# Optimization experiments

Hardware: AMD Instinct MI355X
Metric: run time of the kernel (lower is better)

## Reference

```python
import jax, jax.numpy as jnp
import numpy as np

B, L, D, E = 32, 2048, 1024, 2048

def setup_inputs() -> dict:
    key = jax.random.key(0)
    k1, k2, k3, k4, k5 = jax.random.split(key, 5)
    scale_s = 1.0 / np.sqrt(D)
    scale_h = 1.0 / np.sqrt(E)
    return {
        "dec_hidden": jax.random.normal(k1, (B, D), jnp.float32),
        "enc_outputs": jax.random.normal(k2, (B, L, E), jnp.float32),
        "W_s": jax.random.normal(k3, (D, D), jnp.float32) * scale_s,
        "W_h": jax.random.normal(k4, (D, E), jnp.float32) * scale_h,
        "v": jax.random.normal(k5, (D,), jnp.float32) * scale_s,
    }

def reference(dec_hidden, enc_outputs, W_s, W_h, v):
    # s: [B, D] -- projected decoder state (broadcast over src_len, no repeat)
    s = jnp.einsum('bd,ed->be', dec_hidden, W_s)
    # h: [B, L, D] -- projected encoder outputs
    h = jnp.einsum('ble,de->bld', enc_outputs, W_h)
    # additive scores: v^T tanh(s + h) -> [B, L]
    scores = jnp.einsum('bld,d->bl', jnp.tanh(s[:, None, :] + h), v)
    attn = jax.nn.softmax(scores, axis=1)
    # context: weighted sum of encoder outputs -> [B, E]
    ctx = jnp.einsum('bl,ble->be', attn, enc_outputs)
    return (ctx, attn)
```

## Files before the change

### kernel.cpp

```cpp
#include <hip/hip_runtime.h>
#include <cstdint>
#include <cstddef>

#define B_ 32
#define L_ 2048
#define D_ 1024
#define E_ 2048

typedef __attribute__((ext_vector_type(8))) short short8;
typedef __attribute__((ext_vector_type(16))) float f32x16;
typedef __attribute__((ext_vector_type(4))) unsigned int uint4v;

__device__ __forceinline__ void async_copy16(const void* g, void* l) {
  __builtin_amdgcn_global_load_lds((const __attribute__((address_space(1))) void*)g,
                                   (__attribute__((address_space(3))) void*)l, 16, 0, 0);
}

__device__ __forceinline__ unsigned int pack_bf16_2(float lo, float hi) {
  unsigned int ul = __builtin_bit_cast(unsigned int, lo) + 0x8000u;
  unsigned int uh = __builtin_bit_cast(unsigned int, hi) + 0x8000u;
  return (ul >> 16) | (uh & 0xFFFF0000u);
}

__device__ __forceinline__ float fast_tanh(float x) {
  float e = __expf(2.0f * x);
  return 1.0f - 2.0f / (e + 1.0f);
}

__global__ __launch_bounds__(256) void k_s(const float* __restrict__ dec,
                                           const float* __restrict__ Ws,
                                           float* __restrict__ s) {
  int wid = threadIdx.x >> 6, lane = threadIdx.x & 63;
  int out = blockIdx.x * 4 + wid;
  int b = out >> 10, i = out & 1023;
  const float* dr = dec + b * D_;
  const float* wr = Ws + (size_t)i * D_;
  float acc = 0.f;
#pragma unroll
  for (int c = 0; c < 4; ++c) {
    int d0 = c * 256 + lane * 4;
    float4 x = *(const float4*)(dr + d0);
    float4 w = *(const float4*)(wr + d0);
    acc += x.x * w.x + x.y * w.y + x.z * w.z + x.w * w.w;
  }
#pragma unroll
  for (int off = 32; off >= 1; off >>= 1) acc += __shfl_xor(acc, off, 64);
  if (lane == 0) s[out] = acc;
}

__global__ __launch_bounds__(256) void k_cvt(const float* __restrict__ src,
                                             unsigned short* __restrict__ dst) {
  size_t i = ((size_t)blockIdx.x * 256 + threadIdx.x) * 8;
  float4 a = *(const float4*)(src + i);
  float4 b = *(const float4*)(src + i + 4);
  uint4v p;
  p.x = pack_bf16_2(a.x, a.y);
  p.y = pack_bf16_2(a.z, a.w);
  p.z = pack_bf16_2(b.x, b.y);
  p.w = pack_bf16_2(b.z, b.w);
  *(uint4v*)(dst + i) = p;
}

__global__ __launch_bounds__(256, 3) void k_gemm(const float* __restrict__ enc,
                                                 const unsigned short* __restrict__ whb,
                                                 const float* __restrict__ sbias,
                                                 const float* __restrict__ vvec,
                                                 float* __restrict__ scores) {
  __shared__ alignas(16) float As[128 * 64];
  __shared__ alignas(16) unsigned short Bs[64 * 128];

  const int tid = threadIdx.x;
  const int wid = tid >> 6;
  const int lane = tid & 63;
  const int wm = wid >> 1;
  const int wn = wid & 1;

  const int flat = blockIdx.x;
  const int nt = (flat >> 3) & 7;
  const int mt = (flat & 7) | ((flat >> 6) << 3);
  const int m_base = mt * 128, n_base = nt * 128;
  const int b_idx = m_base >> 11;

  const int rp = lane >> 4;
  const int ul = lane & 15;
  const int u0 = ul ^ rp;
  const float* gA = enc + (size_t)(m_base + wid * 32 + rp) * E_;
  int offA[8];
#pragma unroll
  for (int it = 0; it < 8; ++it)
    offA[it] = it * 4 * E_ + ((u0 ^ ((it & 3) << 2)) << 2);
  const unsigned short* gB = whb + (size_t)n_base * E_;
  int offB[4];
#pragma unroll
  for (int it = 0; it < 4; ++it) {
    int ulog = u0 ^ (it << 2);
    offB[it] = (wid * 32 + it * 8 + 2 * rp + (ulog >> 3)) * E_ + (ulog & 7) * 8;
  }

  const int col = lane & 31;
  const int h = lane >> 5;
  const float* arow[2];
#pragma unroll
  for (int mi = 0; mi < 2; ++mi) arow[mi] = &As[(wm * 64 + mi * 32 + col) * 64];
  int aoff[4][2];
#pragma unroll
  for (int ks = 0; ks < 4; ++ks)
#pragma unroll
    for (int j = 0; j < 2; ++j)
      aoff[ks][j] = ((ks * 4 + h * 2 + j) ^ (col & 15)) * 4;
  const unsigned short* brow[2];
#pragma unroll
  for (int ni = 0; ni < 2; ++ni) brow[ni] = &Bs[(wn * 32 + ni * 16 + (col >> 1)) * 128];
  int boff[4];
#pragma unroll
  for (int ks = 0; ks < 4; ++ks)
    boff[ks] = ((((col & 1) << 3) + ks * 2 + h) ^ ((col >> 1) & 15)) * 8;

  f32x16 acc[2][2] = {};

  for (int kk = 0; kk < E_; kk += 64) {
    __syncthreads();
#pragma unroll
    for (int it = 0; it < 8; ++it)
      async_copy16(gA + offA[it] + kk, &As[(wid * 32 + it * 4) * 64]);
#pragma unroll
    for (int it = 0; it < 4; ++it)
      async_copy16(gB + offB[it] + kk, &Bs[(wid * 16 + it * 4) * 128]);
    __syncthreads();

#pragma unroll
    for (int ks = 0; ks < 4; ++ks) {
      short8 bf[2];
#pragma unroll
      for (int ni = 0; ni < 2; ++ni) bf[ni] = *(const short8*)(brow[ni] + boff[ks]);
#pragma unroll
      for (int mi = 0; mi < 2; ++mi) {
        float4 f0 = *(const float4*)(arow[mi] + aoff[ks][0]);
        float4 f1 = *(const float4*)(arow[mi] + aoff[ks][1]);
        uint4v pa;
        pa.x = pack_bf16_2(f0.x, f0.y);
        pa.y = pack_bf16_2(f0.z, f0.w);
        pa.z = pack_bf16_2(f1.x, f1.y);
        pa.w = pack_bf16_2(f1.z, f1.w);
        short8 af = __builtin_bit_cast(short8, pa);
#pragma unroll
        for (int ni = 0; ni < 2; ++ni)
          acc[mi][ni] = __builtin_amdgcn_mfma_f32_32x32x16_bf16(af, bf[ni], acc[mi][ni], 0, 0, 0);
      }
    }
  }

  float vv[2], sv[2];
#pragma unroll
  for (int ni = 0; ni < 2; ++ni) {
    int n = n_base + wn * 64 + ni * 32 + col;
    vv[ni] = vvec[n];
    sv[ni] = sbias[b_idx * D_ + n];
  }
#pragma unroll
  for (int mi = 0; mi < 2; ++mi) {
#pragma unroll
    for (int reg = 0; reg < 16; ++reg) {
      float sum = 0.f;
#pragma unroll
      for (int ni = 0; ni < 2; ++ni)
        sum += vv[ni] * fast_tanh(sv[ni] + acc[mi][ni][reg]);
      sum += __shfl_xor(sum, 1, 64);
      sum += __shfl_xor(sum, 2, 64);
      sum += __shfl_xor(sum, 4, 64);
      sum += __shfl_xor(sum, 8, 64);
      sum += __shfl_xor(sum, 16, 64);
      if (col == 0)
        atomicAdd(&scores[m_base + wm * 64 + mi * 32 + (reg & 3) + 8 * (reg >> 2) + h * 4], sum);
    }
  }
}

__global__ __launch_bounds__(256) void k_softmax(float* __restrict__ sc) {
  int b = blockIdx.x, tid = threadIdx.x;
  int lane = tid & 63, wid = tid >> 6;
  float* row = sc + (size_t)b * L_;
  float vals[8];
  float mx = -1e30f;
#pragma unroll
  for (int j = 0; j < 8; ++j) { vals[j] = row[tid + j * 256]; mx = fmaxf(mx, vals[j]); }
#pragma unroll
  for (int off = 32; off >= 1; off >>= 1) mx = fmaxf(mx, __shfl_xor(mx, off, 64));
  __shared__ float redm[4], reds[4];
  if (lane == 0) redm[wid] = mx;
  __syncthreads();
  mx = fmaxf(fmaxf(redm[0], redm[1]), fmaxf(redm[2], redm[3]));
  float sum = 0.f;
#pragma unroll
  for (int j = 0; j < 8; ++j) { vals[j] = __expf(vals[j] - mx); sum += vals[j]; }
#pragma unroll
  for (int off = 32; off >= 1; off >>= 1) sum += __shfl_xor(sum, off, 64);
  if (lane == 0) reds[wid] = sum;
  __syncthreads();
  sum = reds[0] + reds[1] + reds[2] + reds[3];
  float inv = 1.0f / sum;
#pragma unroll
  for (int j = 0; j < 8; ++j) row[tid + j * 256] = vals[j] * inv;
}

__global__ __launch_bounds__(256) void k_ctx(const float* __restrict__ enc,
                                             const float* __restrict__ attn,
                                             float* __restrict__ ctx) {
  int b = blockIdx.y;
  int lc = blockIdx.x >> 1;
  int eh = blockIdx.x & 1;
  int t = threadIdx.x;
  __shared__ float aw[64];
  if (t < 64) aw[t] = attn[(size_t)b * L_ + lc * 64 + t];
  __syncthreads();
  const float* base = enc + ((size_t)b * L_ + (size_t)lc * 64) * E_ + eh * 1024;
  float4 a0 = make_float4(0.f, 0.f, 0.f, 0.f);
#pragma unroll 4
  for (int l = 0; l < 64; ++l) {
    float w = aw[l];
    float4 x0 = *(const float4*)(base + (size_t)l * E_ + t * 4);
    a0.x += w * x0.x; a0.y += w * x0.y; a0.z += w * x0.z; a0.w += w * x0.w;
  }
  float* cb = ctx + (size_t)b * E_ + eh * 1024 + t * 4;
  atomicAdd(cb + 0, a0.x);
  atomicAdd(cb + 1, a0.y);
  atomicAdd(cb + 2, a0.z);
  atomicAdd(cb + 3, a0.w);
}

extern "C" void kernel_launch(void* const* d_in, const int* in_sizes, int n_in,
                              void* d_out, int out_size, void* d_ws, size_t ws_size,
                              hipStream_t stream) {
  const float* dec = (const float*)d_in[0];
  const float* enc = (const float*)d_in[1];
  const float* Ws  = (const float*)d_in[2];
  const float* Wh  = (const float*)d_in[3];
  const float* v   = (const float*)d_in[4];

  float* ctx  = (float*)d_out;
  float* attn = (float*)d_out + B_ * E_;

  unsigned short* whb = (unsigned short*)d_ws;
  float* sbuf = (float*)((char*)d_ws + (size_t)D_ * E_ * sizeof(unsigned short));

  hipMemsetAsync(d_out, 0, (size_t)out_size * sizeof(float), stream);

  k_s<<<dim3((B_ * D_) / 4), dim3(256), 0, stream>>>(dec, Ws, sbuf);
  k_cvt<<<dim3((D_ * E_) / (256 * 8)), dim3(256), 0, stream>>>(Wh, whb);
  k_gemm<<<dim3((B_ * L_ / 128) * (D_ / 128)), dim3(256), 0, stream>>>(enc, whb, sbuf, v, attn);
  k_softmax<<<dim3(B_), dim3(256), 0, stream>>>(attn);
  k_ctx<<<dim3(64, B_), dim3(256), 0, stream>>>(enc, attn, ctx);
}
```

Before: 1.111 ms.

## Prefetch A via registers with bf16 conversion before LDS store, double-buffer B

Encoder rows are now loaded into registers one k-step ahead, converted to bf16 with the hardware packed-convert instruction, and written to LDS as bf16. This halves A's LDS footprint and removes the per-MFMA fp32-to-bf16 repacking. W_h tiles are double-buffered in LDS with async copies issued for the next step before the current MFMAs, so global loads overlap compute. In exchange it uses more registers for the prefetched A values, and the conversion switches from manual rounding to the hardware convert.

```diff
diff --git a/kernel.cpp b/kernel.cpp
--- a/kernel.cpp
+++ b/kernel.cpp
@@ -20,6 +20,12 @@
   unsigned int ul = __builtin_bit_cast(unsigned int, lo) + 0x8000u;
   unsigned int uh = __builtin_bit_cast(unsigned int, hi) + 0x8000u;
   return (ul >> 16) | (uh & 0xFFFF0000u);
+}
+
+__device__ __forceinline__ unsigned int cvt_pk_bf16(float lo, float hi) {
+  unsigned int r;
+  asm("v_cvt_pk_bf16_f32 %0, %1, %2" : "=v"(r) : "v"(lo), "v"(hi));
+  return r;
 }
 
 __device__ __forceinline__ float fast_tanh(float x) {
@@ -66,8 +72,8 @@
                                                  const float* __restrict__ sbias,
                                                  const float* __restrict__ vvec,
                                                  float* __restrict__ scores) {
-  __shared__ alignas(16) float As[128 * 64];
-  __shared__ alignas(16) unsigned short Bs[64 * 128];
+  __shared__ alignas(16) unsigned short As[64 * 128];
+  __shared__ alignas(16) unsigned short Bs[2][64 * 128];
 
   const int tid = threadIdx.x;
   const int wid = tid >> 6;
@@ -81,73 +87,94 @@
   const int m_base = mt * 128, n_base = nt * 128;
   const int b_idx = m_base >> 11;
 
+  const int sRow = wid * 32 + (lane >> 1);
+  const int sHf = lane & 1;
+  const float* gA = enc + (size_t)(m_base + sRow) * E_ + sHf * 32;
+  const int sLine = sRow >> 1;
+  int aWoff[4];
+#pragma unroll
+  for (int c2 = 0; c2 < 4; ++c2) {
+    int ul = ((sRow & 1) << 3) + sHf * 4 + c2;
+    aWoff[c2] = sLine * 256 + ((ul ^ (sLine & 15)) << 4);
+  }
+
   const int rp = lane >> 4;
-  const int ul = lane & 15;
-  const int u0 = ul ^ rp;
-  const float* gA = enc + (size_t)(m_base + wid * 32 + rp) * E_;
-  int offA[8];
-#pragma unroll
-  for (int it = 0; it < 8; ++it)
-    offA[it] = it * 4 * E_ + ((u0 ^ ((it & 3) << 2)) << 2);
+  const int u0 = (lane & 15) ^ rp;
   const unsigned short* gB = whb + (size_t)n_base * E_;
-  int offB[4];
+  int offB[4], ldsB[4];
 #pragma unroll
   for (int it = 0; it < 4; ++it) {
     int ulog = u0 ^ (it << 2);
     offB[it] = (wid * 32 + it * 8 + 2 * rp + (ulog >> 3)) * E_ + (ulog & 7) * 8;
+    ldsB[it] = (wid * 16 + it * 4) * 256;
   }
 
   const int col = lane & 31;
   const int h = lane >> 5;
-  const float* arow[2];
-#pragma unroll
-  for (int mi = 0; mi < 2; ++mi) arow[mi] = &As[(wm * 64 + mi * 32 + col) * 64];
-  int aoff[4][2];
+  int soff[4];
 #pragma unroll
   for (int ks = 0; ks < 4; ++ks)
-#pragma unroll
-    for (int j = 0; j < 2; ++j)
-      aoff[ks][j] = ((ks * 4 + h * 2 + j) ^ (col & 15)) * 4;
-  const unsigned short* brow[2];
-#pragma unroll
-  for (int ni = 0; ni < 2; ++ni) brow[ni] = &Bs[(wn * 32 + ni * 16 + (col >> 1)) * 128];
-  int boff[4];
-#pragma unroll
-  for (int ks = 0; ks < 4; ++ks)
-    boff[ks] = ((((col & 1) << 3) + ks * 2 + h) ^ ((col >> 1) & 15)) * 8;
+    soff[ks] = ((((col & 1) << 3) + ks * 2 + h) ^ ((col >> 1) & 15)) << 4;
+  const char* aBase[2];
+#pragma unroll
+  for (int mi = 0; mi < 2; ++mi)
+    aBase[mi] = (const char*)As + (wm * 32 + mi * 16 + (col >> 1)) * 256;
+  const char* bBase[2];
+#pragma unroll
+  for (int ni = 0; ni < 2; ++ni)
+    bBase[ni] = (const char*)Bs + (wn * 32 + ni * 16 + (col >> 1)) * 256;
 
   f32x16 acc[2][2] = {};
-
+  float4 rAv[8];
+
+#pragma unroll
+  for (int it = 0; it < 4; ++it)
+    async_copy16(gB + offB[it], (char*)Bs + ldsB[it]);
+#pragma unroll
+  for (int c = 0; c < 8; ++c)
+    rAv[c] = *(const float4*)(gA + c * 4);
+
+  int bufOff = 0;
   for (int kk = 0; kk < E_; kk += 64) {
+    unsigned int w[16];
+#pragma unroll
+    for (int i = 0; i < 16; ++i) {
+      const float* f = (const float*)&rAv[i >> 1];
+      w[i] = cvt_pk_bf16(f[(i & 1) * 2], f[(i & 1) * 2 + 1]);
+    }
     __syncthreads();
 #pragma unroll
-    for (int it = 0; it < 8; ++it)
-      async_copy16(gA + offA[it] + kk, &As[(wid * 32 + it * 4) * 64]);
-#pragma unroll
-    for (int it = 0; it < 4; ++it)
-      async_copy16(gB + offB[it] + kk, &Bs[(wid * 16 + it * 4) * 128]);
+    for (int c2 = 0; c2 < 4; ++c2) {
+      uint4v q;
+      q.x = w[c2 * 4 + 0]; q.y = w[c2 * 4 + 1];
+      q.z = w[c2 * 4 + 2]; q.w = w[c2 * 4 + 3];
+      *(uint4v*)((char*)As + aWoff[c2]) = q;
+    }
     __syncthreads();
 
+    if (kk + 64 < E_) {
+#pragma unroll
+      for (int it = 0; it < 4; ++it)
+        async_copy16(gB + offB[it] + kk + 64, (char*)Bs + (bufOff ^ 16384) + ldsB[it]);
+#pragma unroll
+      for (int c = 0; c < 8; ++c)
+        rAv[c] = *(const float4*)(gA + kk + 64 + c * 4);
+    }
+
 #pragma unroll
     for (int ks = 0; ks < 4; ++ks) {
-      short8 bf[2];
-#pragma unroll
-      for (int ni = 0; ni < 2; ++ni) bf[ni] = *(const short8*)(brow[ni] + boff[ks]);
-#pragma unroll
-      for (int mi = 0; mi < 2; ++mi) {
-        float4 f0 = *(const float4*)(arow[mi] + aoff[ks][0]);
-        float4 f1 = *(const float4*)(arow[mi] + aoff[ks][1]);
-        uint4v pa;
-        pa.x = pack_bf16_2(f0.x, f0.y);
-        pa.y = pack_bf16_2(f0.z, f0.w);
-        pa.z = pack_bf16_2(f1.x, f1.y);
-        pa.w = pack_bf16_2(f1.z, f1.w);
-        short8 af = __builtin_bit_cast(short8, pa);
+      short8 bf[2], af[2];
+#pragma unroll
+      for (int ni = 0; ni < 2; ++ni) bf[ni] = *(const short8*)(bBase[ni] + bufOff + soff[ks]);
+#pragma unroll
+      for (int mi = 0; mi < 2; ++mi) af[mi] = *(const short8*)(aBase[mi] + soff[ks]);
+#pragma unroll
+      for (int mi = 0; mi < 2; ++mi)
 #pragma unroll
         for (int ni = 0; ni < 2; ++ni)
-          acc[mi][ni] = __builtin_amdgcn_mfma_f32_32x32x16_bf16(af, bf[ni], acc[mi][ni], 0, 0, 0);
-      }
-    }
+          acc[mi][ni] = __builtin_amdgcn_mfma_f32_32x32x16_bf16(af[mi], bf[ni], acc[mi][ni], 0, 0, 0);
+    }
+    bufOff ^= 16384;
   }
 
   float vv[2], sv[2];
```

Result: slower. 1.308 ms (+17.8%).
